# Optimization experiments

Hardware: AMD Instinct MI355X
Metric: run time of the kernel (lower is better)

## Reference

```python
import jax, jax.numpy as jnp
import numpy as np

B, S, T = 8, 2048, 128  # batch, seq_len, token_embedding_dim (== dep_transformed_dim, required by source bug)


def setup_inputs() -> dict:
    key = jax.random.key(0)
    k1, k2, k3, k4, k5, k6, k7 = jax.random.split(key, 7)
    sT = 1.0 / np.sqrt(T)
    sS = 1.0 / np.sqrt(S)
    return {
        "token_embeddings": jax.random.normal(k1, (B, S, T), jnp.float32),
        "dep_embeddings": jax.random.normal(k2, (B, S, T), jnp.float32),  # dead input (source bug), kept for fidelity
        "dep_heads": jax.random.randint(k3, (B, S), 0, S, jnp.int32),
        # composition_transform = Bilinear(T, T, T): weight [T_out, T_in1, T_in2], bias [T_out]
        "W_comp": jax.random.uniform(k4, (T, T, T), jnp.float32, -sT, sT),
        "b_comp": jax.random.uniform(k5, (T,), jnp.float32, -sT, sT),
        # reduction_transform = Linear(S, 1)
        "w_red": jax.random.uniform(k6, (1, S), jnp.float32, -sS, sS),
        "b_red": jax.random.uniform(k7, (1,), jnp.float32, -sS, sS),
    }


def reference(token_embeddings, dep_embeddings, dep_heads, W_comp, b_comp, w_red, b_red):
    # Faithful to source semantics (including the bug where dep_transform output is
    # discarded and tanh is applied to token_embeddings instead):
    #   dense[b,i,j,:] = tanh( bilinear(token[b,j], mask(i==heads[b,j]) * tanh(token[b,j])) )
    #   out[b,i,t]     = sum_j w_red[j] * dense[b,i,j,t] + b_red
    # Where mask is zero, bilinear collapses to its bias, so we never materialize
    # the [B,S,S,T] tensor: compute the 'active' value per token j and scatter-add
    # the delta vs. the bias-only baseline into row i = dep_heads[b,j].
    h = jnp.tanh(token_embeddings)                                   # [B,S,T]
    val = jnp.einsum('bsp,tpq,bsq->bst', token_embeddings, W_comp, h) + b_comp  # [B,S,T]
    act = jnp.tanh(val)                                              # active (masked-in) values
    base_val = jnp.tanh(b_comp)                                      # [T] value where mask is zero
    w = w_red[0]                                                     # [S], reduction weights over j
    base = jnp.sum(w) * base_val + b_red[0]                          # [T] bias-only row
    delta = w[None, :, None] * (act - base_val)                      # [B,S,T]
    b_idx = jnp.arange(token_embeddings.shape[0])[:, None]           # [B,1]
    out = base + jnp.zeros_like(act).at[b_idx, dep_heads].add(delta) # scatter over head rows
    return out
```

## Files before the change

### kernel.cpp

```cpp
#include <hip/hip_runtime.h>
#include <hip/hip_fp16.h>
#include <math.h>

#define S_LEN 2048
#define T_DIM 128
#define BM 128
#define TN 32
#define NBLK 512
#define TOKR 132

typedef _Float16 half8 __attribute__((ext_vector_type(8)));
typedef _Float16 half4 __attribute__((ext_vector_type(4)));
typedef float floatx16 __attribute__((ext_vector_type(16)));

__device__ __forceinline__ float tanh_fast(float x) {
  return 1.0f - __fdividef(2.0f, 1.0f + __expf(2.0f * x));
}

__global__ __launch_bounds__(256) void prep_kernel(
    const float* __restrict__ W, const float* __restrict__ w_red,
    const float* __restrict__ b_comp, const float* __restrict__ b_red,
    _Float16* __restrict__ W16f, float* __restrict__ out) {
  const int blk = blockIdx.x;
  const int tid = threadIdx.x;
  if (blk < 1024) {
    const int t = blk >> 3;
    const int qh = (blk >> 2) & 1;
    const int it = blk & 3;
    const int tc = t >> 5, tl = t & 31;
    const int e8 = it * 256 + tid;
    const int p = e8 >> 3;
    const int q = qh * 64 + (e8 & 7) * 8;
    const float* src = W + (size_t)t * 16384 + (size_t)p * 128 + q;
    const float4 v0 = *(const float4*)src;
    const float4 v1 = *(const float4*)(src + 4);
    half8 h;
    h[0] = (_Float16)v0.x; h[1] = (_Float16)v0.y;
    h[2] = (_Float16)v0.z; h[3] = (_Float16)v0.w;
    h[4] = (_Float16)v1.x; h[5] = (_Float16)v1.y;
    h[6] = (_Float16)v1.z; h[7] = (_Float16)v1.w;
    const int kc = q >> 4, lh2 = (q >> 3) & 1;
    *(half8*)(W16f + ((size_t)((p * 4 + tc) * 8 + kc)) * 512 + lh2 * 256 + tl * 8) = h;
  } else {
    __shared__ float red4[4];
    float part = 0.f;
#pragma unroll
    for (int i = 0; i < 8; ++i) part += w_red[tid * 8 + i];
#pragma unroll
    for (int off = 32; off > 0; off >>= 1) part += __shfl_down(part, off, 64);
    if ((tid & 63) == 0) red4[tid >> 6] = part;
    __syncthreads();
    const float Sw = red4[0] + red4[1] + red4[2] + red4[3];
    const float br = b_red[0];
    const size_t base = (size_t)(blk - 1024) * 1024 + (size_t)tid * 4;
    const int t0 = (int)(base & 127);
    float4 v;
    v.x = Sw * tanh_fast(b_comp[t0 + 0]) + br;
    v.y = Sw * tanh_fast(b_comp[t0 + 1]) + br;
    v.z = Sw * tanh_fast(b_comp[t0 + 2]) + br;
    v.w = Sw * tanh_fast(b_comp[t0 + 3]) + br;
    *(float4*)(out + base) = v;
  }
}

__global__ __launch_bounds__(512, 4) void main_kernel(
    const float* __restrict__ tok, const int* __restrict__ heads,
    const _Float16* __restrict__ W16f, const float* __restrict__ b_comp,
    const float* __restrict__ w_red, float* __restrict__ out) {
  __shared__ _Float16 tokT2[128 * TOKR];
  __shared__ float red[2][128 * TN];

  const int tid = threadIdx.x;
  const int lane = tid & 63;
  const int kh = tid >> 6;
  const int l31 = lane & 31;
  const int lh = lane >> 5;
  const int blk = blockIdx.x;
  const int tq = (blk >> 1) & 3;
  const int mb = ((blk >> 3) << 1) | (blk & 1);
  const size_t tokbase = (size_t)mb * BM * T_DIM;

#pragma unroll
  for (int it = 0; it < 8; ++it) {
    const int f = it * 512 + tid;
    const int m = f >> 5;
    const int p0 = (f & 31) * 4;
    const float4 v = *(const float4*)(tok + tokbase + (size_t)m * 128 + p0);
    const int mi = (m & 31) * 4 + (m >> 5);
    tokT2[(p0 + 0) * TOKR + mi] = (_Float16)v.x;
    tokT2[(p0 + 1) * TOKR + mi] = (_Float16)v.y;
    tokT2[(p0 + 2) * TOKR + mi] = (_Float16)v.z;
    tokT2[(p0 + 3) * TOKR + mi] = (_Float16)v.w;
  }

  half8 h16[4];
#pragma unroll
  for (int mh = 0; mh < 4; ++mh) {
    const int m = mh * 32 + l31;
    const int q0 = kh * 16 + lh * 8;
    const float4 v0 = *(const float4*)(tok + tokbase + (size_t)m * 128 + q0);
    const float4 v1 = *(const float4*)(tok + tokbase + (size_t)m * 128 + q0 + 4);
    h16[mh][0] = (_Float16)tanh_fast(v0.x);
    h16[mh][1] = (_Float16)tanh_fast(v0.y);
    h16[mh][2] = (_Float16)tanh_fast(v0.z);
    h16[mh][3] = (_Float16)tanh_fast(v0.w);
    h16[mh][4] = (_Float16)tanh_fast(v1.x);
    h16[mh][5] = (_Float16)tanh_fast(v1.y);
    h16[mh][6] = (_Float16)tanh_fast(v1.z);
    h16[mh][7] = (_Float16)tanh_fast(v1.w);
  }
  __syncthreads();

  const int off0 = ((tq * 8 + kh) << 9) + lane * 8;

  floatx16 acc[4];
#pragma unroll
  for (int mh = 0; mh < 4; ++mh)
#pragma unroll
    for (int r = 0; r < 16; ++r) acc[mh][r] = 0.f;

  half8 bf0, bf1, bf2, bf3;
  half4 tk0, tk1, tk2, tk3;

  auto loadB = [&](half8& bf, int p) {
    bf = *(const half8*)(W16f + (size_t)p * 16384 + off0);
  };
  auto loadT = [&](half4& tk, int p) {
    tk = *(const half4*)(tokT2 + p * TOKR + l31 * 4);
  };

  auto compute = [&](half8 bf, half4 tk) {
    half8 a0 = h16[0] * tk[0];
    half8 a1 = h16[1] * tk[1];
    half8 a2 = h16[2] * tk[2];
    half8 a3 = h16[3] * tk[3];
    acc[0] = __builtin_amdgcn_mfma_f32_32x32x16_f16(a0, bf, acc[0], 0, 0, 0);
    acc[1] = __builtin_amdgcn_mfma_f32_32x32x16_f16(a1, bf, acc[1], 0, 0, 0);
    acc[2] = __builtin_amdgcn_mfma_f32_32x32x16_f16(a2, bf, acc[2], 0, 0, 0);
    acc[3] = __builtin_amdgcn_mfma_f32_32x32x16_f16(a3, bf, acc[3], 0, 0, 0);
  };

  loadB(bf0, 0);  loadT(tk0, 0);
  loadB(bf1, 1);  loadT(tk1, 1);
  loadB(bf2, 2);  loadT(tk2, 2);
  for (int p = 0; p < 124; p += 4) {
    loadB(bf3, p + 3);  loadT(tk3, p + 3);
    compute(bf0, tk0);
    loadB(bf0, p + 4);  loadT(tk0, p + 4);
    compute(bf1, tk1);
    loadB(bf1, p + 5);  loadT(tk1, p + 5);
    compute(bf2, tk2);
    loadB(bf2, p + 6);  loadT(tk2, p + 6);
    compute(bf3, tk3);
  }
  loadB(bf3, 127);  loadT(tk3, 127);
  compute(bf0, tk0);
  compute(bf1, tk1);
  compute(bf2, tk2);
  compute(bf3, tk3);

  __syncthreads();
  {
    float* R = &red[kh & 1][0];
    const int g = kh >> 1;
#pragma unroll
    for (int phase = 0; phase < 4; ++phase) {
      if (g == phase) {
#pragma unroll
        for (int mh = 0; mh < 4; ++mh)
#pragma unroll
          for (int r = 0; r < 16; ++r) {
            const int m_loc = (r & 3) + 8 * (r >> 2) + 4 * lh;
            const int addr = (mh * 32 + m_loc) * TN + l31;
            if (phase == 0) R[addr] = acc[mh][r];
            else            R[addr] += acc[mh][r];
          }
      }
      __syncthreads();
    }
  }

  const int t_loc = tid & 31;
  const int mgrp = tid >> 5;
  const int t = tq * 32 + t_loc;
  const float bc = b_comp[t];
  const float tb = tanh_fast(bc);
#pragma unroll 4
  for (int mi = 0; mi < 8; ++mi) {
    const int m_loc = mi * 16 + mgrp;
    const int gm = mb * BM + m_loc;
    const int head = heads[gm];
    const float wr = w_red[gm & 2047];
    const float v = red[0][m_loc * TN + t_loc] + red[1][m_loc * TN + t_loc] + bc;
    atomicAdd(out + ((size_t)(gm >> 11) * S_LEN + head) * T_DIM + t,
              wr * (tanh_fast(v) - tb));
  }
}

extern "C" void kernel_launch(void* const* d_in, const int* in_sizes, int n_in,
                              void* d_out, int out_size, void* d_ws, size_t ws_size,
                              hipStream_t stream) {
  const float* tok    = (const float*)d_in[0];
  const int*   heads  = (const int*)d_in[2];
  const float* W      = (const float*)d_in[3];
  const float* b_comp = (const float*)d_in[4];
  const float* w_red  = (const float*)d_in[5];
  const float* b_red  = (const float*)d_in[6];
  float* out = (float*)d_out;

  _Float16* W16f = (_Float16*)d_ws;

  prep_kernel<<<3072, 256, 0, stream>>>(W, w_red, b_comp, b_red, W16f, out);
  main_kernel<<<NBLK, 512, 0, stream>>>(tok, heads, W16f, b_comp, w_red, out);
}
```

Before: 159.0 us.

## Fuse weight-conversion prep into main kernel with grid-wide atomic barrier

Merges the prep kernel (fp32→fp16 weight relayout, bias-row init of the output) into the main kernel. Each of the 512 blocks converts its share of W and writes part of the output baseline, then signals a global counter. It spins on that counter before the MFMA loop, and the token staging is overlapped with the wait. This removes a kernel launch and its tail, but adds a memset and relies on all 512 blocks being co-resident, which risks deadlock if occupancy drops.

```diff
diff --git a/kernel.cpp b/kernel.cpp
--- a/kernel.cpp
+++ b/kernel.cpp
@@ -17,58 +17,15 @@
   return 1.0f - __fdividef(2.0f, 1.0f + __expf(2.0f * x));
 }
 
-__global__ __launch_bounds__(256) void prep_kernel(
-    const float* __restrict__ W, const float* __restrict__ w_red,
-    const float* __restrict__ b_comp, const float* __restrict__ b_red,
-    _Float16* __restrict__ W16f, float* __restrict__ out) {
-  const int blk = blockIdx.x;
-  const int tid = threadIdx.x;
-  if (blk < 1024) {
-    const int t = blk >> 3;
-    const int qh = (blk >> 2) & 1;
-    const int it = blk & 3;
-    const int tc = t >> 5, tl = t & 31;
-    const int e8 = it * 256 + tid;
-    const int p = e8 >> 3;
-    const int q = qh * 64 + (e8 & 7) * 8;
-    const float* src = W + (size_t)t * 16384 + (size_t)p * 128 + q;
-    const float4 v0 = *(const float4*)src;
-    const float4 v1 = *(const float4*)(src + 4);
-    half8 h;
-    h[0] = (_Float16)v0.x; h[1] = (_Float16)v0.y;
-    h[2] = (_Float16)v0.z; h[3] = (_Float16)v0.w;
-    h[4] = (_Float16)v1.x; h[5] = (_Float16)v1.y;
-    h[6] = (_Float16)v1.z; h[7] = (_Float16)v1.w;
-    const int kc = q >> 4, lh2 = (q >> 3) & 1;
-    *(half8*)(W16f + ((size_t)((p * 4 + tc) * 8 + kc)) * 512 + lh2 * 256 + tl * 8) = h;
-  } else {
-    __shared__ float red4[4];
-    float part = 0.f;
-#pragma unroll
-    for (int i = 0; i < 8; ++i) part += w_red[tid * 8 + i];
-#pragma unroll
-    for (int off = 32; off > 0; off >>= 1) part += __shfl_down(part, off, 64);
-    if ((tid & 63) == 0) red4[tid >> 6] = part;
-    __syncthreads();
-    const float Sw = red4[0] + red4[1] + red4[2] + red4[3];
-    const float br = b_red[0];
-    const size_t base = (size_t)(blk - 1024) * 1024 + (size_t)tid * 4;
-    const int t0 = (int)(base & 127);
-    float4 v;
-    v.x = Sw * tanh_fast(b_comp[t0 + 0]) + br;
-    v.y = Sw * tanh_fast(b_comp[t0 + 1]) + br;
-    v.z = Sw * tanh_fast(b_comp[t0 + 2]) + br;
-    v.w = Sw * tanh_fast(b_comp[t0 + 3]) + br;
-    *(float4*)(out + base) = v;
-  }
-}
-
-__global__ __launch_bounds__(512, 4) void main_kernel(
+__global__ __launch_bounds__(512, 4) void fused_kernel(
     const float* __restrict__ tok, const int* __restrict__ heads,
-    const _Float16* __restrict__ W16f, const float* __restrict__ b_comp,
-    const float* __restrict__ w_red, float* __restrict__ out) {
+    const float* __restrict__ W, const float* __restrict__ b_comp,
+    const float* __restrict__ w_red, const float* __restrict__ b_red,
+    _Float16* __restrict__ W16f, int* __restrict__ counter,
+    float* __restrict__ out) {
   __shared__ _Float16 tokT2[128 * TOKR];
   __shared__ float red[2][128 * TN];
+  __shared__ float swred[8];
 
   const int tid = threadIdx.x;
   const int lane = tid & 63;
@@ -79,6 +36,60 @@
   const int tq = (blk >> 1) & 3;
   const int mb = ((blk >> 3) << 1) | (blk & 1);
   const size_t tokbase = (size_t)mb * BM * T_DIM;
+
+  {
+    const float4 wv = *(const float4*)(w_red + tid * 4);
+    float part = wv.x + wv.y + wv.z + wv.w;
+#pragma unroll
+    for (int o = 32; o > 0; o >>= 1) part += __shfl_down(part, o, 64);
+    if (lane == 0) swred[kh] = part;
+
+    {
+      const int task = blk * 2 + (tid >> 8);
+      const int t = task >> 3;
+      const int qh = (task >> 2) & 1;
+      const int it = task & 3;
+      const int tc = t >> 5, tl = t & 31;
+      const int tid8 = tid & 255;
+      const int e8 = it * 256 + tid8;
+      const int p = e8 >> 3;
+      const int q = qh * 64 + (e8 & 7) * 8;
+      const float* src = W + (size_t)t * 16384 + (size_t)p * 128 + q;
+      const float4 v0 = *(const float4*)src;
+      const float4 v1 = *(const float4*)(src + 4);
+      half8 h;
+      h[0] = (_Float16)v0.x; h[1] = (_Float16)v0.y;
+      h[2] = (_Float16)v0.z; h[3] = (_Float16)v0.w;
+      h[4] = (_Float16)v1.x; h[5] = (_Float16)v1.y;
+      h[6] = (_Float16)v1.z; h[7] = (_Float16)v1.w;
+      const int kc = q >> 4, lh2 = (q >> 3) & 1;
+      *(half8*)(W16f + ((size_t)((p * 4 + tc) * 8 + kc)) * 512 + lh2 * 256 + tl * 8) = h;
+    }
+
+    __syncthreads();
+    float Sw = 0.f;
+#pragma unroll
+    for (int w = 0; w < 8; ++w) Sw += swred[w];
+    const float br = b_red[0];
+
+    const size_t base = (size_t)blk * 4096 + (size_t)tid * 8;
+    const int t0 = (int)(base & 127);
+    float4 a, b;
+    a.x = Sw * tanh_fast(b_comp[t0 + 0]) + br;
+    a.y = Sw * tanh_fast(b_comp[t0 + 1]) + br;
+    a.z = Sw * tanh_fast(b_comp[t0 + 2]) + br;
+    a.w = Sw * tanh_fast(b_comp[t0 + 3]) + br;
+    b.x = Sw * tanh_fast(b_comp[t0 + 4]) + br;
+    b.y = Sw * tanh_fast(b_comp[t0 + 5]) + br;
+    b.z = Sw * tanh_fast(b_comp[t0 + 6]) + br;
+    b.w = Sw * tanh_fast(b_comp[t0 + 7]) + br;
+    *(float4*)(out + base) = a;
+    *(float4*)(out + base + 4) = b;
+  }
+
+  __threadfence();
+  __syncthreads();
+  if (tid == 0) atomicAdd(counter, 1);
 
 #pragma unroll
   for (int it = 0; it < 8; ++it) {
@@ -109,7 +120,15 @@
     h16[mh][6] = (_Float16)tanh_fast(v1.z);
     h16[mh][7] = (_Float16)tanh_fast(v1.w);
   }
+
+  if (tid == 0) {
+    while (__hip_atomic_load(counter, __ATOMIC_RELAXED,
+                             __HIP_MEMORY_SCOPE_AGENT) < NBLK) {
+      __builtin_amdgcn_s_sleep(8);
+    }
+  }
   __syncthreads();
+  __threadfence();
 
   const int off0 = ((tq * 8 + kh) << 9) + lane * 8;
 
@@ -208,8 +227,11 @@
   const float* b_red  = (const float*)d_in[6];
   float* out = (float*)d_out;
 
-  _Float16* W16f = (_Float16*)d_ws;
-
-  prep_kernel<<<3072, 256, 0, stream>>>(W, w_red, b_comp, b_red, W16f, out);
-  main_kernel<<<NBLK, 512, 0, stream>>>(tok, heads, W16f, b_comp, w_red, out);
+  char* ws = (char*)d_ws;
+  _Float16* W16f = (_Float16*)ws;
+  int* counter   = (int*)(ws + (12u << 20));
+
+  hipMemsetAsync(counter, 0, sizeof(int), stream);
+  fused_kernel<<<NBLK, 512, 0, stream>>>(tok, heads, W, b_comp, w_red, b_red,
+                                         W16f, counter, out);
 }
```

Result: slower. 355.5 us (+123.6%).

## Reshape block tile to 64 rows by 64 output columns

Applied to the files above, without the earlier changes.

Changes each block's tile from 128 tokens x 32 outputs to 64 tokens x 64 outputs. Each wave now issues two B-fragment loads per p step and reuses each A operand across two MFMAs, so A-operand construction is halved, while the W16 global traffic per block doubles across fewer tokens. The software pipeline moves from 4-deep to 3-deep buffering, and the LDS footprint for the transposed tokens shrinks. The block count and grid mapping are unchanged.

```diff
diff --git a/kernel.cpp b/kernel.cpp
--- a/kernel.cpp
+++ b/kernel.cpp
@@ -4,13 +4,13 @@
 
 #define S_LEN 2048
 #define T_DIM 128
-#define BM 128
-#define TN 32
+#define BM 64
+#define TN 64
 #define NBLK 512
-#define TOKR 132
+#define TOKR 66
 
 typedef _Float16 half8 __attribute__((ext_vector_type(8)));
-typedef _Float16 half4 __attribute__((ext_vector_type(4)));
+typedef _Float16 half2t __attribute__((ext_vector_type(2)));
 typedef float floatx16 __attribute__((ext_vector_type(16)));
 
 __device__ __forceinline__ float tanh_fast(float x) {
@@ -68,7 +68,7 @@
     const _Float16* __restrict__ W16f, const float* __restrict__ b_comp,
     const float* __restrict__ w_red, float* __restrict__ out) {
   __shared__ _Float16 tokT2[128 * TOKR];
-  __shared__ float red[2][128 * TN];
+  __shared__ float red[2][BM * TN];
 
   const int tid = threadIdx.x;
   const int lane = tid & 63;
@@ -76,26 +76,26 @@
   const int l31 = lane & 31;
   const int lh = lane >> 5;
   const int blk = blockIdx.x;
-  const int tq = (blk >> 1) & 3;
-  const int mb = ((blk >> 3) << 1) | (blk & 1);
+  const int th = (blk >> 1) & 1;
+  const int mb = ((blk >> 2) << 1) | (blk & 1);
   const size_t tokbase = (size_t)mb * BM * T_DIM;
 
 #pragma unroll
-  for (int it = 0; it < 8; ++it) {
+  for (int it = 0; it < 4; ++it) {
     const int f = it * 512 + tid;
     const int m = f >> 5;
     const int p0 = (f & 31) * 4;
     const float4 v = *(const float4*)(tok + tokbase + (size_t)m * 128 + p0);
-    const int mi = (m & 31) * 4 + (m >> 5);
+    const int mi = (m & 31) * 2 + (m >> 5);
     tokT2[(p0 + 0) * TOKR + mi] = (_Float16)v.x;
     tokT2[(p0 + 1) * TOKR + mi] = (_Float16)v.y;
     tokT2[(p0 + 2) * TOKR + mi] = (_Float16)v.z;
     tokT2[(p0 + 3) * TOKR + mi] = (_Float16)v.w;
   }
 
-  half8 h16[4];
-#pragma unroll
-  for (int mh = 0; mh < 4; ++mh) {
+  half8 h16[2];
+#pragma unroll
+  for (int mh = 0; mh < 2; ++mh) {
     const int m = mh * 32 + l31;
     const int q0 = kh * 16 + lh * 8;
     const float4 v0 = *(const float4*)(tok + tokbase + (size_t)m * 128 + q0);
@@ -111,53 +111,52 @@
   }
   __syncthreads();
 
-  const int off0 = ((tq * 8 + kh) << 9) + lane * 8;
-
-  floatx16 acc[4];
-#pragma unroll
-  for (int mh = 0; mh < 4; ++mh)
-#pragma unroll
-    for (int r = 0; r < 16; ++r) acc[mh][r] = 0.f;
-
-  half8 bf0, bf1, bf2, bf3;
-  half4 tk0, tk1, tk2, tk3;
-
-  auto loadB = [&](half8& bf, int p) {
-    bf = *(const half8*)(W16f + (size_t)p * 16384 + off0);
+  int off[2];
+#pragma unroll
+  for (int tt = 0; tt < 2; ++tt)
+    off[tt] = (((th * 2 + tt) * 8 + kh) << 9) + lane * 8;
+
+  floatx16 acc[2][2];
+#pragma unroll
+  for (int mh = 0; mh < 2; ++mh)
+#pragma unroll
+    for (int tt = 0; tt < 2; ++tt)
+#pragma unroll
+      for (int r = 0; r < 16; ++r) acc[mh][tt][r] = 0.f;
+
+  half8 bf0[2], bf1[2], bf2[2];
+  half2t tk0, tk1, tk2;
+
+  auto loadB = [&](half8 (&bf)[2], int p) {
+    const _Float16* wp = W16f + (size_t)p * 16384;
+    bf[0] = *(const half8*)(wp + off[0]);
+    bf[1] = *(const half8*)(wp + off[1]);
   };
-  auto loadT = [&](half4& tk, int p) {
-    tk = *(const half4*)(tokT2 + p * TOKR + l31 * 4);
+  auto loadT = [&](half2t& tk, int p) {
+    tk = *(const half2t*)(tokT2 + p * TOKR + l31 * 2);
   };
 
-  auto compute = [&](half8 bf, half4 tk) {
+  auto compute = [&](half8 (&bf)[2], half2t tk) {
     half8 a0 = h16[0] * tk[0];
     half8 a1 = h16[1] * tk[1];
-    half8 a2 = h16[2] * tk[2];
-    half8 a3 = h16[3] * tk[3];
-    acc[0] = __builtin_amdgcn_mfma_f32_32x32x16_f16(a0, bf, acc[0], 0, 0, 0);
-    acc[1] = __builtin_amdgcn_mfma_f32_32x32x16_f16(a1, bf, acc[1], 0, 0, 0);
-    acc[2] = __builtin_amdgcn_mfma_f32_32x32x16_f16(a2, bf, acc[2], 0, 0, 0);
-    acc[3] = __builtin_amdgcn_mfma_f32_32x32x16_f16(a3, bf, acc[3], 0, 0, 0);
+    acc[0][0] = __builtin_amdgcn_mfma_f32_32x32x16_f16(a0, bf[0], acc[0][0], 0, 0, 0);
+    acc[0][1] = __builtin_amdgcn_mfma_f32_32x32x16_f16(a0, bf[1], acc[0][1], 0, 0, 0);
+    acc[1][0] = __builtin_amdgcn_mfma_f32_32x32x16_f16(a1, bf[0], acc[1][0], 0, 0, 0);
+    acc[1][1] = __builtin_amdgcn_mfma_f32_32x32x16_f16(a1, bf[1], acc[1][1], 0, 0, 0);
   };
 
   loadB(bf0, 0);  loadT(tk0, 0);
   loadB(bf1, 1);  loadT(tk1, 1);
-  loadB(bf2, 2);  loadT(tk2, 2);
-  for (int p = 0; p < 124; p += 4) {
-    loadB(bf3, p + 3);  loadT(tk3, p + 3);
+  for (int p = 0; p < 126; p += 3) {
+    loadB(bf2, p + 2);  loadT(tk2, p + 2);
     compute(bf0, tk0);
-    loadB(bf0, p + 4);  loadT(tk0, p + 4);
+    loadB(bf0, p + 3);  loadT(tk0, p + 3);
     compute(bf1, tk1);
-    loadB(bf1, p + 5);  loadT(tk1, p + 5);
+    loadB(bf1, p + 4);  loadT(tk1, p + 4);
     compute(bf2, tk2);
-    loadB(bf2, p + 6);  loadT(tk2, p + 6);
-    compute(bf3, tk3);
-  }
-  loadB(bf3, 127);  loadT(tk3, 127);
+  }
   compute(bf0, tk0);
   compute(bf1, tk1);
-  compute(bf2, tk2);
-  compute(bf3, tk3);
 
   __syncthreads();
   {
@@ -167,27 +166,31 @@
     for (int phase = 0; phase < 4; ++phase) {
       if (g == phase) {
 #pragma unroll
-        for (int mh = 0; mh < 4; ++mh)
-#pragma unroll
-          for (int r = 0; r < 16; ++r) {
-            const int m_loc = (r & 3) + 8 * (r >> 2) + 4 * lh;
-            const int addr = (mh * 32 + m_loc) * TN + l31;
-            if (phase == 0) R[addr] = acc[mh][r];
-            else            R[addr] += acc[mh][r];
+        for (int mh = 0; mh < 2; ++mh)
+#pragma unroll
+          for (int tt = 0; tt < 2; ++tt) {
+            const int t_loc = tt * 32 + l31;
+#pragma unroll
+            for (int r = 0; r < 16; ++r) {
+              const int m_loc = mh * 32 + (r & 3) + 8 * (r >> 2) + 4 * lh;
+              const int addr = m_loc * TN + t_loc;
+              if (phase == 0) R[addr] = acc[mh][tt][r];
+              else            R[addr] += acc[mh][tt][r];
+            }
           }
       }
       __syncthreads();
     }
   }
 
-  const int t_loc = tid & 31;
-  const int mgrp = tid >> 5;
-  const int t = tq * 32 + t_loc;
+  const int t_loc = tid & 63;
+  const int mgrp = tid >> 6;
+  const int t = th * 64 + t_loc;
   const float bc = b_comp[t];
   const float tb = tanh_fast(bc);
 #pragma unroll 4
   for (int mi = 0; mi < 8; ++mi) {
-    const int m_loc = mi * 16 + mgrp;
+    const int m_loc = mi * 8 + mgrp;
     const int gm = mb * BM + m_loc;
     const int head = heads[gm];
     const float wr = w_red[gm & 2047];
```

Result: faster. 155.7 us (-2.1%).
